# Kernel optimization log

Hardware: AMD Instinct MI355X
Metric: run time of the kernel (lower is better)

The kernel has to match this reference:

```python
import jax, jax.numpy as jnp
import numpy as np

B, S, E, H = 4, 1024, 1024, 16
D = E // H          # head_dim = 64
F = 4 * E           # mlp inner = 4096
EPS = 1e-5


def _layernorm(x, scale, bias):
    mu = jnp.mean(x, axis=-1, keepdims=True)
    var = jnp.var(x, axis=-1, keepdims=True)
    return (x - mu) * jax.lax.rsqrt(var + EPS) * scale + bias


def setup_inputs() -> dict:
    key = jax.random.key(0)
    ks = jax.random.split(key, 8)
    std = 0.02
    return {
        "hidden_states": jax.random.normal(ks[0], (B, S, E), jnp.float32),
        "ln1_scale": jnp.ones((E,), jnp.float32),
        "ln1_bias": jnp.zeros((E,), jnp.float32),
        # Conv1D kernels stored as (out_features, in_features), applied as x @ k.T
        "w_attn": jax.random.normal(ks[1], (3 * E, E), jnp.float32) * std,
        "b_attn": jnp.zeros((3 * E,), jnp.float32),
        "w_proj": jax.random.normal(ks[2], (E, E), jnp.float32) * std,
        "b_proj": jnp.zeros((E,), jnp.float32),
        "ln2_scale": jnp.ones((E,), jnp.float32),
        "ln2_bias": jnp.zeros((E,), jnp.float32),
        "w_fc": jax.random.normal(ks[3], (F, E), jnp.float32) * std,
        "b_fc": jnp.zeros((F,), jnp.float32),
        "w_proj2": jax.random.normal(ks[4], (E, F), jnp.float32) * std,
        "b_proj2": jnp.zeros((E,), jnp.float32),
    }


def reference(hidden_states, ln1_scale, ln1_bias, w_attn, b_attn, w_proj, b_proj,
              ln2_scale, ln2_bias, w_fc, b_fc, w_proj2, b_proj2):
    x = hidden_states
    # --- attention sub-block ---
    h = _layernorm(x, ln1_scale, ln1_bias)
    qkv = h @ w_attn.T + b_attn                      # [B,S,3E]
    q, k, v = jnp.split(qkv, 3, axis=2)
    q = q.reshape(B, S, H, D) / jnp.sqrt(jnp.float32(D))
    k = k.reshape(B, S, H, D)
    v = v.reshape(B, S, H, D)
    # NOTE: source sets attention_bias = None, so NO causal mask is applied.
    logits = jnp.einsum("bqhd,bkhd->bhqk", q, k)     # [B,H,S,S]
    attn = jax.nn.softmax(logits, axis=-1)
    o = jnp.einsum("bhqk,bkhd->bqhd", attn, v).reshape(B, S, E)
    o = o @ w_proj.T + b_proj
    x = x + o
    # --- mlp sub-block ---
    h = _layernorm(x, ln2_scale, ln2_bias)
    m = jax.nn.gelu(h @ w_fc.T + b_fc, approximate=True)  # gelu_new
    m = m @ w_proj2.T + b_proj2
    return x + m
```

## Files before the change

kernel.cpp:

```cpp
#include <hip/hip_runtime.h>

#define DEV __device__ __forceinline__

using bf16x8 = __attribute__((ext_vector_type(8))) __bf16;
using f32x4  = __attribute__((ext_vector_type(4))) float;
typedef unsigned int u32;
typedef unsigned short u16;
typedef unsigned long long u64;

static constexpr int Bb = 4, Ss = 1024, Ee = 1024, Hh = 16, Dd = 64, Ff = 4096;
static constexpr int Mm = Bb * Ss;

DEV u16 f2bf(float f) {
  union { float f; u32 u; } v; v.f = f;
  u32 r = v.u + 0x7fffu + ((v.u >> 16) & 1u);
  return (u16)(r >> 16);
}

DEV void gload16(const void* g, void* lds) {
  __builtin_amdgcn_global_load_lds(
      (const __attribute__((address_space(1))) void*)(u64)g,
      (__attribute__((address_space(3))) void*)(u32)(u64)lds,
      16, 0, 0);
}

DEV float gelu_tanh(float x) {
  float x3 = x * x * x;
  float t  = tanhf(0.7978845608028654f * (x + 0.044715f * x3));
  return 0.5f * x * (1.0f + t);
}

DEV int swz(int row, int col) { return row * 64 + (col ^ ((row & 7) << 3)); }

DEV f32x4 MFMA(bf16x8 a, bf16x8 b, f32x4 c) {
  return __builtin_amdgcn_mfma_f32_16x16x32_bf16(a, b, c, 0, 0, 0);
}

__global__ __launch_bounds__(256) void cvt_bf16(const float* __restrict__ in,
                                                u16* __restrict__ out, int n) {
  int i = (blockIdx.x * 256 + threadIdx.x) * 8;
  if (i >= n) return;
  float4 a = *(const float4*)(in + i);
  float4 b = *(const float4*)(in + i + 4);
  uint4 o;
  o.x = (u32)f2bf(a.x) | ((u32)f2bf(a.y) << 16);
  o.y = (u32)f2bf(a.z) | ((u32)f2bf(a.w) << 16);
  o.z = (u32)f2bf(b.x) | ((u32)f2bf(b.y) << 16);
  o.w = (u32)f2bf(b.z) | ((u32)f2bf(b.w) << 16);
  *(uint4*)(out + i) = o;
}

__global__ __launch_bounds__(256) void ln_kernel(const float* __restrict__ x,
                                                 const float* __restrict__ scale,
                                                 const float* __restrict__ bias,
                                                 u16* __restrict__ h) {
  const int row = blockIdx.x, tid = threadIdx.x;
  const float4 v = ((const float4*)(x + (size_t)row * Ee))[tid];
  float s  = v.x + v.y + v.z + v.w;
  float ss = v.x * v.x + v.y * v.y + v.z * v.z + v.w * v.w;
  for (int m = 1; m < 64; m <<= 1) {
    s  += __shfl_xor(s, m, 64);
    ss += __shfl_xor(ss, m, 64);
  }
  __shared__ float red[8];
  const int w = tid >> 6, ln = tid & 63;
  if (ln == 0) { red[w * 2] = s; red[w * 2 + 1] = ss; }
  __syncthreads();
  s  = red[0] + red[2] + red[4] + red[6];
  ss = red[1] + red[3] + red[5] + red[7];
  const float mu   = s * (1.0f / Ee);
  const float var  = ss * (1.0f / Ee) - mu * mu;
  const float rstd = rsqrtf(var + 1e-5f);
  const float4 sc = ((const float4*)scale)[tid];
  const float4 bi = ((const float4*)bias)[tid];
  ushort4 o;
  o.x = f2bf((v.x - mu) * rstd * sc.x + bi.x);
  o.y = f2bf((v.y - mu) * rstd * sc.y + bi.y);
  o.z = f2bf((v.z - mu) * rstd * sc.z + bi.z);
  o.w = f2bf((v.w - mu) * rstd * sc.w + bi.w);
  ((ushort4*)(h + (size_t)row * Ee))[tid] = o;
}

template <int EPI, int AM, int AN>
__global__ __launch_bounds__(256, 5) void gemm3(
    const u16* __restrict__ A, const u16* __restrict__ Bw,
    const float* __restrict__ bias, const float* __restrict__ resid,
    float* __restrict__ outf, u16* __restrict__ outb,
    u16* __restrict__ q, u16* __restrict__ k, u16* __restrict__ v,
    int N, int K) {
  constexpr int BM = AM * 32, BN = AN * 32;
  constexpr int GA = BM / 64, GB = BN / 64;
  __shared__ u16 As[2][BM * 32];
  __shared__ u16 Bs[2][BN * 32];
  const int tid = threadIdx.x;
  const int w = tid >> 6, ln = tid & 63;
  const int lr = ln & 15, lg = ln >> 4;
  const int wr = w >> 1, wc = w & 1;

  const int nwg = gridDim.x * gridDim.y;
  const int bid = blockIdx.y * gridDim.x + blockIdx.x;
  const int sid = (bid & 7) * (nwg >> 3) + (bid >> 3);
  const int bx = sid % gridDim.x, by = sid / gridDim.x;
  const int tm = by * BM, tn = bx * BN;

  f32x4 acc[AM][AN];
  f32x4 zero4 = {0.f, 0.f, 0.f, 0.f};
#pragma unroll
  for (int i = 0; i < AM; ++i)
#pragma unroll
    for (int j = 0; j < AN; ++j) acc[i][j] = zero4;

  const int r0 = tid >> 2;
  const int cs = ((tid & 3) ^ (r0 & 3)) * 8;
  const u16* aP[GA];
  const u16* bP[GB];
#pragma unroll
  for (int i = 0; i < GA; ++i) aP[i] = A + (size_t)(tm + r0 + i * 64) * K + cs;
#pragma unroll
  for (int i = 0; i < GB; ++i) bP[i] = Bw + (size_t)(tn + r0 + i * 64) * K + cs;

  auto STAGE = [&](int buf, int k0) {
#pragma unroll
    for (int i = 0; i < GA; ++i)
      gload16(aP[i] + k0, &As[buf][(tid + i * 256) * 8]);
#pragma unroll
    for (int i = 0; i < GB; ++i)
      gload16(bP[i] + k0, &Bs[buf][(tid + i * 256) * 8]);
  };

  const int fsl = (lg ^ (lr & 3)) << 3;
  const int nt = K >> 5;
  STAGE(0, 0);
  asm volatile("s_waitcnt vmcnt(0)" ::: "memory");
  __builtin_amdgcn_s_barrier();

  for (int t = 0; t < nt; ++t) {
    if (t + 1 < nt) STAGE((t + 1) & 1, (t + 1) << 5);
    const u16* Ab = &As[t & 1][0];
    const u16* Bbuf = &Bs[t & 1][0];
    bf16x8 af[AM], bf[AN];
#pragma unroll
    for (int mi = 0; mi < AM; ++mi)
      af[mi] = *(const bf16x8*)&Ab[(wr * AM * 16 + mi * 16 + lr) * 32 + fsl];
#pragma unroll
    for (int ni = 0; ni < AN; ++ni)
      bf[ni] = *(const bf16x8*)&Bbuf[(wc * AN * 16 + ni * 16 + lr) * 32 + fsl];
#pragma unroll
    for (int mi = 0; mi < AM; ++mi)
#pragma unroll
      for (int ni = 0; ni < AN; ++ni)
        acc[mi][ni] = MFMA(af[mi], bf[ni], acc[mi][ni]);
    asm volatile("s_waitcnt vmcnt(0)" ::: "memory");
    __builtin_amdgcn_s_barrier();
  }

#pragma unroll
  for (int mi = 0; mi < AM; ++mi) {
#pragma unroll
    for (int ni = 0; ni < AN; ++ni) {
      const int gc = tn + wc * AN * 16 + ni * 16 + lr;
#pragma unroll
      for (int j = 0; j < 4; ++j) {
        const int gr = tm + wr * AM * 16 + mi * 16 + lg * 4 + j;
        float val = acc[mi][ni][j] + bias[gc];
        if constexpr (EPI == 0) {
          const int which = gc >> 10, hh = (gc >> 6) & 15, dd = gc & 63;
          const int bb2 = gr >> 10, ss2 = gr & 1023;
          const size_t dst = ((size_t)(bb2 * 16 + hh) * 1024 + ss2) * 64 + dd;
          if (which == 0)      q[dst] = f2bf(val * 0.125f);
          else if (which == 1) k[dst] = f2bf(val);
          else                 v[dst] = f2bf(val);
        } else if constexpr (EPI == 1) {
          const size_t idx = (size_t)gr * N + gc;
          outf[idx] = val + resid[idx];
        } else {
          outb[(size_t)gr * N + gc] = f2bf(gelu_tanh(val));
        }
      }
    }
  }
}

__global__ __launch_bounds__(256) void attn_kernel(const u16* __restrict__ qg,
                                                   const u16* __restrict__ kg,
                                                   const u16* __restrict__ vg,
                                                   u16* __restrict__ ao) {
  __shared__ u16 Qs[64 * 64], Ks[64 * 64], Vt[64 * 64], Ps[64 * 64];
  const int tid = threadIdx.x;
  const int w = tid >> 6, ln = tid & 63;
  const int lr = ln & 15, lg = ln >> 4;
  const int bh = blockIdx.y;
  const int q0 = blockIdx.x * 64;
  const size_t head = (size_t)bh * (Ss * Dd);

  {
    const u16* src = qg + head + (size_t)q0 * Dd;
#pragma unroll
    for (int i = 0; i < 2; ++i) {
      const int gi = i * 256 + tid, row = gi >> 3, g = gi & 7;
      *(uint4*)&Qs[row * 64 + ((g ^ (row & 7)) << 3)] = *(const uint4*)(src + gi * 8);
    }
  }

  f32x4 zero4 = {0.f, 0.f, 0.f, 0.f};
  f32x4 acc_o[4] = {zero4, zero4, zero4, zero4};
  float mrow[4] = {-1e30f, -1e30f, -1e30f, -1e30f};
  float lrow[4] = {0.f, 0.f, 0.f, 0.f};

  for (int kt = 0; kt < 16; ++kt) {
    __syncthreads();
    const u16* ksrc = kg + head + (size_t)kt * 64 * Dd;
    const u16* vsrc = vg + head + (size_t)kt * 64 * Dd;
#pragma unroll
    for (int i = 0; i < 2; ++i) {
      const int gi = i * 256 + tid, row = gi >> 3, g = gi & 7;
      *(uint4*)&Ks[row * 64 + ((g ^ (row & 7)) << 3)] = *(const uint4*)(ksrc + gi * 8);
    }
#pragma unroll
    for (int i = 0; i < 2; ++i) {
      const int kv = i * 32 + (tid >> 3), d0 = (tid & 7) * 8;
      uint4 dv = *(const uint4*)(vsrc + (size_t)kv * Dd + d0);
      const u16* pv = (const u16*)&dv;
#pragma unroll
      for (int j = 0; j < 8; ++j) {
        const int dd = d0 + j;
        Vt[dd * 64 + (((kv >> 3) ^ (dd & 7)) << 3) + (kv & 7)] = pv[j];
      }
    }
    __syncthreads();

    bf16x8 aq[2];
#pragma unroll
    for (int kk = 0; kk < 2; ++kk)
      aq[kk] = *(const bf16x8*)&Qs[swz(w * 16 + lr, kk * 32 + lg * 8)];
    f32x4 sa[4];
#pragma unroll
    for (int kf = 0; kf < 4; ++kf) {
      f32x4 s = zero4;
#pragma unroll
      for (int kk = 0; kk < 2; ++kk) {
        bf16x8 bk = *(const bf16x8*)&Ks[swz(kf * 16 + lr, kk * 32 + lg * 8)];
        s = MFMA(aq[kk], bk, s);
      }
      sa[kf] = s;
    }

#pragma unroll
    for (int j = 0; j < 4; ++j) {
      float mx = fmaxf(fmaxf(sa[0][j], sa[1][j]), fmaxf(sa[2][j], sa[3][j]));
      mx = fmaxf(mx, __shfl_xor(mx, 1, 64));
      mx = fmaxf(mx, __shfl_xor(mx, 2, 64));
      mx = fmaxf(mx, __shfl_xor(mx, 4, 64));
      mx = fmaxf(mx, __shfl_xor(mx, 8, 64));
      const float nm = fmaxf(mrow[j], mx);
      const float corr = __expf(mrow[j] - nm);
      mrow[j] = nm;
      float ssum = 0.f;
#pragma unroll
      for (int kf = 0; kf < 4; ++kf) {
        const float p = __expf(sa[kf][j] - nm);
        sa[kf][j] = p;
        ssum += p;
      }
      ssum += __shfl_xor(ssum, 1, 64);
      ssum += __shfl_xor(ssum, 2, 64);
      ssum += __shfl_xor(ssum, 4, 64);
      ssum += __shfl_xor(ssum, 8, 64);
      lrow[j] = lrow[j] * corr + ssum;
#pragma unroll
      for (int df = 0; df < 4; ++df) acc_o[df][j] *= corr;
    }

#pragma unroll
    for (int kf = 0; kf < 4; ++kf)
#pragma unroll
      for (int j = 0; j < 4; ++j)
        Ps[swz(w * 16 + lg * 4 + j, kf * 16 + lr)] = f2bf(sa[kf][j]);

    __syncthreads();

    bf16x8 ap[2];
#pragma unroll
    for (int kk = 0; kk < 2; ++kk)
      ap[kk] = *(const bf16x8*)&Ps[swz(w * 16 + lr, kk * 32 + lg * 8)];
#pragma unroll
    for (int df = 0; df < 4; ++df) {
#pragma unroll
      for (int kk = 0; kk < 2; ++kk) {
        bf16x8 bv = *(const bf16x8*)&Vt[swz(df * 16 + lr, kk * 32 + lg * 8)];
        acc_o[df] = MFMA(ap[kk], bv, acc_o[df]);
      }
    }
  }

  const int b = bh >> 4, h = bh & 15;
#pragma unroll
  for (int df = 0; df < 4; ++df) {
#pragma unroll
    for (int j = 0; j < 4; ++j) {
      const int srow = q0 + w * 16 + lg * 4 + j;
      const int e = h * 64 + df * 16 + lr;
      ao[((size_t)b * Ss + srow) * Ee + e] = f2bf(acc_o[df][j] / lrow[j]);
    }
  }
}

extern "C" void kernel_launch(void* const* d_in, const int* in_sizes, int n_in,
                              void* d_out, int out_size, void* d_ws, size_t ws_size,
                              hipStream_t stream) {
  const float* x      = (const float*)d_in[0];
  const float* ln1_s  = (const float*)d_in[1];
  const float* ln1_b  = (const float*)d_in[2];
  const float* w_attn = (const float*)d_in[3];
  const float* b_attn = (const float*)d_in[4];
  const float* w_proj = (const float*)d_in[5];
  const float* b_proj = (const float*)d_in[6];
  const float* ln2_s  = (const float*)d_in[7];
  const float* ln2_b  = (const float*)d_in[8];
  const float* w_fc   = (const float*)d_in[9];
  const float* b_fc   = (const float*)d_in[10];
  const float* w_proj2= (const float*)d_in[11];
  const float* b_proj2= (const float*)d_in[12];
  float* out = (float*)d_out;

  char* base = (char*)d_ws;
  size_t off = 0;
  auto alloc = [&](size_t bytes) { char* p = base + off; off += bytes; return p; };
  u16* wA   = (u16*)alloc((size_t)3 * Ee * Ee * 2);
  u16* wP   = (u16*)alloc((size_t)Ee * Ee * 2);
  u16* wF   = (u16*)alloc((size_t)Ff * Ee * 2);
  u16* wP2  = (u16*)alloc((size_t)Ee * Ff * 2);
  u16* h1   = (u16*)alloc((size_t)Mm * Ee * 2);
  u16* qws  = (u16*)alloc((size_t)Mm * Ee * 2);
  u16* kws  = (u16*)alloc((size_t)Mm * Ee * 2);
  u16* vws  = (u16*)alloc((size_t)Mm * Ee * 2);
  u16* aws  = (u16*)alloc((size_t)Mm * Ee * 2);
  float* x1 = (float*)alloc((size_t)Mm * Ee * 4);
  u16* mfc  = qws;

  cvt_bf16<<<3 * Ee * Ee / 2048, 256, 0, stream>>>(w_attn, wA, 3 * Ee * Ee);
  cvt_bf16<<<Ee * Ee / 2048, 256, 0, stream>>>(w_proj, wP, Ee * Ee);
  cvt_bf16<<<Ff * Ee / 2048, 256, 0, stream>>>(w_fc, wF, Ff * Ee);
  cvt_bf16<<<Ee * Ff / 2048, 256, 0, stream>>>(w_proj2, wP2, Ee * Ff);

  ln_kernel<<<Mm, 256, 0, stream>>>(x, ln1_s, ln1_b, h1);
  gemm3<0, 4, 2><<<dim3(48, 32), 256, 0, stream>>>(h1, wA, b_attn, nullptr,
                                                   nullptr, nullptr, qws, kws, vws,
                                                   3 * Ee, Ee);
  attn_kernel<<<dim3(16, 64), 256, 0, stream>>>(qws, kws, vws, aws);
  gemm3<1, 2, 2><<<dim3(16, 64), 256, 0, stream>>>(aws, wP, b_proj, x,
                                                   x1, nullptr, nullptr, nullptr, nullptr,
                                                   Ee, Ee);
  ln_kernel<<<Mm, 256, 0, stream>>>(x1, ln2_s, ln2_b, h1);
  gemm3<2, 4, 2><<<dim3(64, 32), 256, 0, stream>>>(h1, wF, b_fc, nullptr,
                                                   nullptr, mfc, nullptr, nullptr, nullptr,
                                                   Ff, Ee);
  gemm3<1, 2, 2><<<dim3(16, 64), 256, 0, stream>>>(mfc, wP2, b_proj2, x1,
                                                   out, nullptr, nullptr, nullptr, nullptr,
                                                   Ee, Ff);
}
```

Measured before the change: 307.1 us.

## Double-buffer V tile and read Q/K fragments directly from global in attention

The attention kernel now loads Q and K MFMA fragments straight from global memory into registers instead of staging them in shared memory. V is double-buffered in shared memory: the next tile is prefetched into registers and transposed into the alternate buffer after the PV MFMAs, which removes one barrier per iteration. The transposed-store order is rotated per thread to spread LDS bank conflicts. The GEMM launch bound also rises to 6 waves per SIMD, which may force register spills. Direct global K reads depend on L1/L2 hits, since each block rereads K rows across its waves.

Result: slower. 342.6 us (+11.6%).

```diff
diff --git a/kernel.cpp b/kernel.cpp
--- a/kernel.cpp
+++ b/kernel.cpp
@@ -82,7 +82,7 @@
 }
 
 template <int EPI, int AM, int AN>
-__global__ __launch_bounds__(256, 5) void gemm3(
+__global__ __launch_bounds__(256, 6) void gemm3(
     const u16* __restrict__ A, const u16* __restrict__ Bw,
     const float* __restrict__ bias, const float* __restrict__ resid,
     float* __restrict__ outf, u16* __restrict__ outb,
@@ -181,11 +181,12 @@
   }
 }
 
-__global__ __launch_bounds__(256) void attn_kernel(const u16* __restrict__ qg,
-                                                   const u16* __restrict__ kg,
-                                                   const u16* __restrict__ vg,
-                                                   u16* __restrict__ ao) {
-  __shared__ u16 Qs[64 * 64], Ks[64 * 64], Vt[64 * 64], Ps[64 * 64];
+__global__ __launch_bounds__(256) void attn2(const u16* __restrict__ qg,
+                                             const u16* __restrict__ kg,
+                                             const u16* __restrict__ vg,
+                                             u16* __restrict__ ao) {
+  __shared__ u16 Vt[2][64 * 64];
+  __shared__ u16 Ps[64 * 64];
   const int tid = threadIdx.x;
   const int w = tid >> 6, ln = tid & 63;
   const int lr = ln & 15, lg = ln >> 4;
@@ -193,14 +194,34 @@
   const int q0 = blockIdx.x * 64;
   const size_t head = (size_t)bh * (Ss * Dd);
 
+  bf16x8 aq[2];
   {
-    const u16* src = qg + head + (size_t)q0 * Dd;
-#pragma unroll
-    for (int i = 0; i < 2; ++i) {
-      const int gi = i * 256 + tid, row = gi >> 3, g = gi & 7;
-      *(uint4*)&Qs[row * 64 + ((g ^ (row & 7)) << 3)] = *(const uint4*)(src + gi * 8);
-    }
-  }
+    const u16* qrow = qg + head + (size_t)(q0 + w * 16 + lr) * Dd;
+    aq[0] = *(const bf16x8*)(qrow + lg * 8);
+    aq[1] = *(const bf16x8*)(qrow + 32 + lg * 8);
+  }
+
+  const int kv0 = tid >> 3;
+  const int dsel = tid & 7, d0 = dsel * 8;
+
+  auto VSTORE = [&](int buf, uint4 dv, int kv) {
+    const u16* pv = (const u16*)&dv;
+#pragma unroll
+    for (int jj = 0; jj < 8; ++jj) {
+      const int j = (jj + dsel) & 7;
+      const int dd = d0 + j;
+      Vt[buf][dd * 64 + (kv & 7) + (((kv >> 3) ^ (dd & 7)) << 3)] = pv[j];
+    }
+  };
+
+  {
+    const u16* vsrc = vg + head;
+    uint4 a = *(const uint4*)(vsrc + (size_t)kv0 * Dd + d0);
+    uint4 b = *(const uint4*)(vsrc + (size_t)(32 + kv0) * Dd + d0);
+    VSTORE(0, a, kv0);
+    VSTORE(0, b, 32 + kv0);
+  }
+  __syncthreads();
 
   f32x4 zero4 = {0.f, 0.f, 0.f, 0.f};
   f32x4 acc_o[4] = {zero4, zero4, zero4, zero4};
@@ -208,40 +229,26 @@
   float lrow[4] = {0.f, 0.f, 0.f, 0.f};
 
   for (int kt = 0; kt < 16; ++kt) {
-    __syncthreads();
-    const u16* ksrc = kg + head + (size_t)kt * 64 * Dd;
-    const u16* vsrc = vg + head + (size_t)kt * 64 * Dd;
-#pragma unroll
-    for (int i = 0; i < 2; ++i) {
-      const int gi = i * 256 + tid, row = gi >> 3, g = gi & 7;
-      *(uint4*)&Ks[row * 64 + ((g ^ (row & 7)) << 3)] = *(const uint4*)(ksrc + gi * 8);
-    }
-#pragma unroll
-    for (int i = 0; i < 2; ++i) {
-      const int kv = i * 32 + (tid >> 3), d0 = (tid & 7) * 8;
-      uint4 dv = *(const uint4*)(vsrc + (size_t)kv * Dd + d0);
-      const u16* pv = (const u16*)&dv;
-#pragma unroll
-      for (int j = 0; j < 8; ++j) {
-        const int dd = d0 + j;
-        Vt[dd * 64 + (((kv >> 3) ^ (dd & 7)) << 3) + (kv & 7)] = pv[j];
-      }
-    }
-    __syncthreads();
-
-    bf16x8 aq[2];
-#pragma unroll
-    for (int kk = 0; kk < 2; ++kk)
-      aq[kk] = *(const bf16x8*)&Qs[swz(w * 16 + lr, kk * 32 + lg * 8)];
+    const int cur = kt & 1, nc = cur ^ 1;
+    const bool more = (kt + 1) < 16;
+
+    uint4 dv0, dv1;
+    if (more) {
+      const u16* vnxt = vg + head + (size_t)(kt + 1) * 64 * Dd;
+      dv0 = *(const uint4*)(vnxt + (size_t)kv0 * Dd + d0);
+      dv1 = *(const uint4*)(vnxt + (size_t)(32 + kv0) * Dd + d0);
+    }
+
+    const u16* kbase = kg + head + (size_t)kt * 64 * Dd;
     f32x4 sa[4];
 #pragma unroll
     for (int kf = 0; kf < 4; ++kf) {
+      const u16* krow = kbase + (size_t)(kf * 16 + lr) * Dd;
+      bf16x8 bk0 = *(const bf16x8*)(krow + lg * 8);
+      bf16x8 bk1 = *(const bf16x8*)(krow + 32 + lg * 8);
       f32x4 s = zero4;
-#pragma unroll
-      for (int kk = 0; kk < 2; ++kk) {
-        bf16x8 bk = *(const bf16x8*)&Ks[swz(kf * 16 + lr, kk * 32 + lg * 8)];
-        s = MFMA(aq[kk], bk, s);
-      }
+      s = MFMA(aq[0], bk0, s);
+      s = MFMA(aq[1], bk1, s);
       sa[kf] = s;
     }
 
@@ -287,10 +294,16 @@
     for (int df = 0; df < 4; ++df) {
 #pragma unroll
       for (int kk = 0; kk < 2; ++kk) {
-        bf16x8 bv = *(const bf16x8*)&Vt[swz(df * 16 + lr, kk * 32 + lg * 8)];
+        bf16x8 bv = *(const bf16x8*)&Vt[cur][swz(df * 16 + lr, kk * 32 + lg * 8)];
         acc_o[df] = MFMA(ap[kk], bv, acc_o[df]);
       }
     }
+
+    if (more) {
+      VSTORE(nc, dv0, kv0);
+      VSTORE(nc, dv1, 32 + kv0);
+    }
+    __syncthreads();
   }
 
   const int b = bh >> 4, h = bh & 15;
@@ -347,7 +360,7 @@
   gemm3<0, 4, 2><<<dim3(48, 32), 256, 0, stream>>>(h1, wA, b_attn, nullptr,
                                                    nullptr, nullptr, qws, kws, vws,
                                                    3 * Ee, Ee);
-  attn_kernel<<<dim3(16, 64), 256, 0, stream>>>(qws, kws, vws, aws);
+  attn2<<<dim3(16, 64), 256, 0, stream>>>(qws, kws, vws, aws);
   gemm3<1, 2, 2><<<dim3(16, 64), 256, 0, stream>>>(aws, wP, b_proj, x,
                                                    x1, nullptr, nullptr, nullptr, nullptr,
                                                    Ee, Ee);
```
